# Kernel optimization log

Measured on AMD Instinct MI355X. Metric: run time of the kernel, lower is better.

## Reference

```python
import jax, jax.numpy as jnp
import numpy as np

EPS = 1e-12  # torch F.normalize default eps


def conv1x1(x, w, b):
    # x: [N,C,H,W], w: [O,C], b: [O]
    return jnp.einsum('nchw,oc->nohw', x, w) + b[None, :, None, None]


def forward_sa(f1, f2, cw1, cb1, cw2, cb2):
    c1 = conv1x1(f1, cw1, cb1)  # [N,1,H,W]
    c2 = conv1x1(f2, cw2, cb2)
    n, _, h, w = c1.shape
    c1 = jax.nn.softmax(c1.reshape(n, 1, h * w), axis=-1).reshape(n, 1, h, w)
    c2 = jax.nn.softmax(c2.reshape(n, 1, h * w), axis=-1).reshape(n, 1, h, w)
    return c1 * f1, c2 * f2


def l2_normalize_ch(x):
    # F.normalize(x): L2 over channel dim (dim=1), norm clamped to eps
    n = jnp.sqrt(jnp.sum(x * x, axis=1, keepdims=True))
    return x / jnp.maximum(n, EPS)


def forward_ca(f1, f2, pw1, pb1, pw2, pb2):
    N, C, H, W = f1.shape
    HW = H * W
    f1_cl = conv1x1(f1, pw1, pb1).reshape(N, -1, HW)  # [N,Cl,HW]
    f2_cl = conv1x1(f2, pw2, pb2).reshape(N, -1, HW)
    # A = f2_cl^T @ f1_cl : [N,HW,HW]
    A_c = jnp.tanh(jnp.einsum('nci,ncj->nij', f2_cl, f1_cl))
    f1_v = f1.reshape(N, C, HW)
    f2_v = f2.reshape(N, C, HW)
    # f1_hat = f1_v @ A_c^T ; f2_hat = f2_v @ A_c
    f1_hat = jnp.einsum('ncj,nij->nci', f1_v, A_c).reshape(N, C, H, W)
    f2_hat = jnp.einsum('ncj,nji->nci', f2_v, A_c).reshape(N, C, H, W)
    return l2_normalize_ch(f1_hat), l2_normalize_ch(f2_hat)


def setup_inputs() -> dict:
    key = jax.random.key(0)
    ks = jax.random.split(key, 10)
    N, C, H, W = 8, 256, 32, 32
    Cl = C // 16
    return {
        'f1': jax.random.normal(ks[0], (N, C, H, W), jnp.float32),
        'f2': jax.random.normal(ks[1], (N, C, H, W), jnp.float32),
        'pw1': jax.random.normal(ks[2], (Cl, C), jnp.float32) * 0.05,
        'pb1': jax.random.normal(ks[3], (Cl,), jnp.float32) * 0.05,
        'pw2': jax.random.normal(ks[4], (Cl, C), jnp.float32) * 0.05,
        'pb2': jax.random.normal(ks[5], (Cl,), jnp.float32) * 0.05,
        'cw1': jax.random.normal(ks[6], (1, C), jnp.float32) * 0.05,
        'cb1': jax.random.normal(ks[7], (1,), jnp.float32) * 0.05,
        'cw2': jax.random.normal(ks[8], (1, C), jnp.float32) * 0.05,
        'cb2': jax.random.normal(ks[9], (1,), jnp.float32) * 0.05,
    }


def reference(f1, f2, pw1, pb1, pw2, pb2, cw1, cb1, cw2, cb2):
    fp1, fp2 = f1, f2
    for i in range(5):
        s1, s2 = forward_sa(fp1, fp2, cw1, cb1, cw2, cb2)
        h1, h2 = forward_ca(s1, s2, pw1, pb1, pw2, pb2)
        if i < 4:
            fp1 = jax.nn.relu(h1 + fp1)
            fp2 = jax.nn.relu(h2 + fp2)
    return h1, h2, s1, s2
```

## Files before the change

### kernel.cpp

```cpp
#include <hip/hip_runtime.h>
#include <cstdint>
#include <cstddef>

#define N_  8
#define C_  256
#define HW_ 1024
#define CL_ 16
#define SZ_ (N_*C_*HW_)
#define WSCALE_ 4096.0f

typedef __attribute__((ext_vector_type(8))) _Float16 half8;
typedef __attribute__((ext_vector_type(4))) float f32x4;

static __device__ __forceinline__ float tanh_fast(float x){
  x = fminf(fmaxf(x, -15.f), 15.f);
  float e = __expf(2.f * x);
  return (e - 1.f) / (e + 1.f);
}

static __device__ __forceinline__ unsigned short f2h(float x){
  _Float16 h = (_Float16)x;
  return *(unsigned short*)&h;
}

static __device__ __forceinline__ void combine16(
    const float* __restrict__ mpart, const float* __restrict__ spart,
    int base, float& m, float& rl)
{
  m = -1e30f;
  #pragma unroll
  for (int k = 0; k < 16; ++k) m = fmaxf(m, mpart[base * 16 + k]);
  float s = 0.f;
  #pragma unroll
  for (int k = 0; k < 16; ++k) s += spart[base * 16 + k] * __expf(mpart[base * 16 + k] - m);
  rl = 1.f / s;
}

#define GLD16(g, l) __builtin_amdgcn_global_load_lds( \
    (const __attribute__((address_space(1))) void*)(g), \
    (__attribute__((address_space(3))) void*)(l), 16, 0, 0)

#define WAITV(N) asm volatile("s_waitcnt vmcnt(" #N ")" ::: "memory")

__global__ __launch_bounds__(256) void k_sa_dot(
    const float* __restrict__ fp1, const float* __restrict__ fp2,
    const float* __restrict__ cw1, const float* __restrict__ cw2,
    const float* __restrict__ pw1, const float* __restrict__ pw2,
    float* __restrict__ cval, float* __restrict__ pdot,
    float* __restrict__ mpart, float* __restrict__ spart,
    _Float16* __restrict__ fh1, _Float16* __restrict__ fh2)
{
  const int bid = blockIdx.x;
  const int n = bid & 7, r = bid >> 3;
  const int side = r >> 4, hw0 = (r & 15) * 64;
  const int t = threadIdx.x, hwl = t & 63, cg = t >> 6;
  const float* __restrict__ pw = side ? pw2 : pw1;
  const float* __restrict__ cw = side ? cw2 : cw1;
  const float* __restrict__ f  = (side ? fp2 : fp1) + (size_t)n * C_ * HW_ + hw0 + hwl;
  _Float16* __restrict__ fh = (side ? fh2 : fh1) + (size_t)n * C_ * HW_ + hw0 + hwl;
  const int cb = __builtin_amdgcn_readfirstlane(cg * 64);

  float acc[17];
  #pragma unroll
  for (int l = 0; l < 17; ++l) acc[l] = 0.f;

  for (int cc = 0; cc < 64; ++cc){
    const int c = cb + cc;
    const float v = f[(size_t)c * HW_];
    fh[(size_t)c * HW_] = (_Float16)v;
    acc[16] += v * cw[c];
    #pragma unroll
    for (int l = 0; l < 16; ++l) acc[l] += v * pw[l * C_ + c];
  }

  __shared__ float red[17][4][64];
  #pragma unroll
  for (int l = 0; l < 17; ++l) red[l][cg][hwl] = acc[l];
  __syncthreads();

  if (t < 64){
    const int base = n * 2 + side;
    float xc = 0.f;
    #pragma unroll
    for (int l = 0; l < 17; ++l){
      const float s = red[l][0][t] + red[l][1][t] + red[l][2][t] + red[l][3][t];
      if (l < 16) pdot[((size_t)base * CL_ + l) * HW_ + hw0 + t] = s;
      else      { cval[(size_t)base * HW_ + hw0 + t] = s; xc = s; }
    }
    float mb = xc;
    #pragma unroll
    for (int off = 32; off; off >>= 1) mb = fmaxf(mb, __shfl_xor(mb, off));
    float e = __expf(xc - mb);
    #pragma unroll
    for (int off = 32; off; off >>= 1) e += __shfl_xor(e, off);
    if (t == 0){
      mpart[base * 16 + (hw0 >> 6)] = mb;
      spart[base * 16 + (hw0 >> 6)] = e;
    }
  }
}

__global__ __launch_bounds__(256) void k_corr(
    const float* __restrict__ cval, const float* __restrict__ pdot,
    const float* __restrict__ pb1, const float* __restrict__ pb2,
    const float* __restrict__ mpart, const float* __restrict__ spart,
    unsigned short* __restrict__ Abf, unsigned short* __restrict__ Atbf)
{
  const int bid = blockIdx.x;
  const int n = bid & 7, r4i = bid >> 3;
  const int i0 = (r4i >> 4) * 64, j0 = (r4i & 15) * 64;
  const int b1 = n * 2, b2 = n * 2 + 1;
  __align__(16) __shared__ float s2[CL_][64];
  __align__(16) __shared__ float s1[CL_][64];
  __shared__ unsigned short at_s[64][68];
  const int t = threadIdx.x;
  const int lr = t >> 4, lc = (t & 15) * 4;

  float m1, rl1, m2, rl2;
  combine16(mpart, spart, b1, m1, rl1);
  combine16(mpart, spart, b2, m2, rl2);

  {
    const float bias2 = pb2[lr];
    const float4 c2 = *(const float4*)&cval[(size_t)b2 * HW_ + i0 + lc];
    const float4 p2 = *(const float4*)&pdot[((size_t)b2 * CL_ + lr) * HW_ + i0 + lc];
    s2[lr][lc + 0] = __expf(c2.x - m2) * rl2 * p2.x + bias2;
    s2[lr][lc + 1] = __expf(c2.y - m2) * rl2 * p2.y + bias2;
    s2[lr][lc + 2] = __expf(c2.z - m2) * rl2 * p2.z + bias2;
    s2[lr][lc + 3] = __expf(c2.w - m2) * rl2 * p2.w + bias2;

    const float bias1 = pb1[lr];
    const float4 c1 = *(const float4*)&cval[(size_t)b1 * HW_ + j0 + lc];
    const float4 p1 = *(const float4*)&pdot[((size_t)b1 * CL_ + lr) * HW_ + j0 + lc];
    s1[lr][lc + 0] = __expf(c1.x - m1) * rl1 * p1.x + bias1;
    s1[lr][lc + 1] = __expf(c1.y - m1) * rl1 * p1.y + bias1;
    s1[lr][lc + 2] = __expf(c1.z - m1) * rl1 * p1.z + bias1;
    s1[lr][lc + 3] = __expf(c1.w - m1) * rl1 * p1.w + bias1;
  }
  __syncthreads();

  const int ti = t >> 4, tj = t & 15;
  float acc[4][4];
  #pragma unroll
  for (int a = 0; a < 4; ++a)
    #pragma unroll
    for (int b = 0; b < 4; ++b) acc[a][b] = 0.f;

  #pragma unroll
  for (int l = 0; l < CL_; ++l){
    const float4 a4 = *(const float4*)&s2[l][ti * 4];
    const float4 b4 = *(const float4*)&s1[l][tj * 4];
    const float av[4] = {a4.x, a4.y, a4.z, a4.w};
    const float bv[4] = {b4.x, b4.y, b4.z, b4.w};
    #pragma unroll
    for (int a = 0; a < 4; ++a)
      #pragma unroll
      for (int b = 0; b < 4; ++b) acc[a][b] += av[a] * bv[b];
  }

  float tf[4][4];
  #pragma unroll
  for (int a = 0; a < 4; ++a)
    #pragma unroll
    for (int b = 0; b < 4; ++b) tf[a][b] = tanh_fast(acc[a][b]);

  float w1j[4], w2i[4];
  #pragma unroll
  for (int b = 0; b < 4; ++b)
    w1j[b] = WSCALE_ * __expf(cval[(size_t)b1 * HW_ + j0 + tj * 4 + b] - m1) * rl1;
  #pragma unroll
  for (int a = 0; a < 4; ++a)
    w2i[a] = WSCALE_ * __expf(cval[(size_t)b2 * HW_ + i0 + ti * 4 + a] - m2) * rl2;

  unsigned short* __restrict__ An  = Abf  + ((size_t)n << 20);
  unsigned short* __restrict__ Atn = Atbf + ((size_t)n << 20);
  #pragma unroll
  for (int a = 0; a < 4; ++a){
    ushort4 va;
    va.x = f2h(tf[a][0] * w1j[0]); va.y = f2h(tf[a][1] * w1j[1]);
    va.z = f2h(tf[a][2] * w1j[2]); va.w = f2h(tf[a][3] * w1j[3]);
    *(ushort4*)&An[(size_t)(i0 + ti * 4 + a) * HW_ + j0 + tj * 4] = va;
  }
  #pragma unroll
  for (int b = 0; b < 4; ++b){
    ushort4 vb;
    vb.x = f2h(tf[0][b] * w2i[0]); vb.y = f2h(tf[1][b] * w2i[1]);
    vb.z = f2h(tf[2][b] * w2i[2]); vb.w = f2h(tf[3][b] * w2i[3]);
    *(ushort4*)&at_s[tj * 4 + b][ti * 4] = vb;
  }
  __syncthreads();
  #pragma unroll
  for (int rep = 0; rep < 2; ++rep){
    const int idx = t + rep * 256;
    const int r = idx >> 3, q = (idx & 7) * 8;
    const ushort4 lo = *(const ushort4*)&at_s[r][q];
    const ushort4 hi = *(const ushort4*)&at_s[r][q + 4];
    *(ushort4*)&Atn[(size_t)(j0 + r) * HW_ + i0 + q] = lo;
    *(ushort4*)&Atn[(size_t)(j0 + r) * HW_ + i0 + q + 4] = hi;
  }
}

__global__ __launch_bounds__(512, 4) void k_gemm_fused(
    const _Float16* __restrict__ fhc1, const _Float16* __restrict__ fhc2,
    const unsigned short* __restrict__ Abf, const unsigned short* __restrict__ Atbf,
    const float* __restrict__ fpin1, const float* __restrict__ fpin2,
    float* __restrict__ fpo1, float* __restrict__ fpo2,
    _Float16* __restrict__ fhn1, _Float16* __restrict__ fhn2,
    const float* __restrict__ pw1, const float* __restrict__ pw2,
    const float* __restrict__ cw1, const float* __restrict__ cw2,
    float* __restrict__ cval, float* __restrict__ pdot,
    float* __restrict__ mpart, float* __restrict__ spart,
    float* __restrict__ out, int last)
{
  const int bid = blockIdx.x;
  const int n = bid & 7, r2 = bid >> 3;
  const int g = r2 >> 4, i0 = (r2 & 15) * 64;
  const unsigned short* __restrict__ X =
      (const unsigned short*)((g ? fhc2 : fhc1) + (size_t)n * C_ * HW_);
  const unsigned short* __restrict__ B = (g ? Atbf : Abf) + ((size_t)n << 20);

  __shared__ __align__(16) unsigned char pool[61440];

  const int t = threadIdx.x, w = t >> 6, l = t & 63;
  const int wr = w >> 1, wc = w & 1;

  f32x4 acc[4][2];
  #pragma unroll
  for (int fm = 0; fm < 4; ++fm)
    #pragma unroll
    for (int fn = 0; fn < 2; ++fn)
      acc[fm][fn] = (f32x4){0.f, 0.f, 0.f, 0.f};

  auto stage = [&](int buf, int k0){
    unsigned short* Xsb = (unsigned short*)(pool + buf * 16384);
    #pragma unroll
    for (int s = 0; s < 2; ++s){
      const int q = (w * 2 + s) * 64 + l;
      const int row = q >> 2;
      const int kc = (q & 3) ^ (row & 3);
      GLD16(X + (size_t)row * HW_ + k0 + kc * 8, &Xsb[(w * 2 + s) * 512]);
    }
    if (w < 4){
      unsigned short* Bsb = (unsigned short*)(pool + 49152 + buf * 4096);
      const int q = w * 64 + l;
      const int row = q >> 2;
      const int kc = (q & 3) ^ (row & 3);
      GLD16(B + (size_t)(i0 + row) * HW_ + k0 + kc * 8, &Bsb[w * 512]);
    }
  };

  stage(0, 0);
  stage(1, 32);
  stage(2, 64);

  int cur = 0;
  for (int kt = 0; kt < 32; ++kt){
    const int rem = (31 - kt) < 2 ? (31 - kt) : 2;
    if (w < 4){
      if (rem == 2)      WAITV(6);
      else if (rem == 1) WAITV(3);
      else               WAITV(0);
    } else {
      if (rem == 2)      WAITV(4);
      else if (rem == 1) WAITV(2);
      else               WAITV(0);
    }
    __builtin_amdgcn_sched_barrier(0);
    __builtin_amdgcn_s_barrier();

    const unsigned short* Xsb = (const unsigned short*)(pool + cur * 16384);
    const unsigned short* Bsb = (const unsigned short*)(pool + 49152 + cur * 4096);
    half8 a[4], bb[2];
    #pragma unroll
    for (int fm = 0; fm < 4; ++fm){
      const int row = wr * 64 + fm * 16 + (l & 15);
      const int kc = (l >> 4) ^ (row & 3);
      a[fm] = *(const half8*)&Xsb[row * 32 + kc * 8];
    }
    #pragma unroll
    for (int fn = 0; fn < 2; ++fn){
      const int row = wc * 32 + fn * 16 + (l & 15);
      const int kc = (l >> 4) ^ (row & 3);
      bb[fn] = *(const half8*)&Bsb[row * 32 + kc * 8];
    }
    #pragma unroll
    for (int fm = 0; fm < 4; ++fm)
      #pragma unroll
      for (int fn = 0; fn < 2; ++fn)
        acc[fm][fn] = __builtin_amdgcn_mfma_f32_16x16x32_f16(a[fm], bb[fn], acc[fm][fn], 0, 0, 0);

    asm volatile("s_waitcnt lgkmcnt(0)" ::: "memory");
    __builtin_amdgcn_sched_barrier(0);
    __builtin_amdgcn_s_barrier();
    __builtin_amdgcn_sched_barrier(0);

    if (kt < 29) stage(cur, (kt + 3) * 32);
    cur = (cur == 2) ? 0 : cur + 1;
  }

  float* pwT   = (float*)pool;
  float* redp  = (float*)(pool + 20480);
  float* ssred = (float*)(pool + 55296);
  float* rinvp = (float*)(pool + 56320);

  float ss0 = 0.f, ss1 = 0.f;
  #pragma unroll
  for (int fm = 0; fm < 4; ++fm)
    #pragma unroll
    for (int r = 0; r < 4; ++r){
      ss0 += acc[fm][0][r] * acc[fm][0][r];
      ss1 += acc[fm][1][r] * acc[fm][1][r];
    }
  ss0 += __shfl_xor(ss0, 16); ss0 += __shfl_xor(ss0, 32);
  ss1 += __shfl_xor(ss1, 16); ss1 += __shfl_xor(ss1, 32);
  if (l < 16){
    ssred[wr * 64 + wc * 32 + l]      = ss0;
    ssred[wr * 64 + wc * 32 + 16 + l] = ss1;
  }

  if (!last){
    const float* __restrict__ pw = g ? pw2 : pw1;
    const float* __restrict__ cw = g ? cw2 : cw1;
    {
      const int idx = t * 8;
      const int lq = idx >> 8, c = idx & 255;
      const float4 p0 = *(const float4*)&pw[lq * C_ + c];
      const float4 p1 = *(const float4*)&pw[lq * C_ + c + 4];
      pwT[(c + 0) * 20 + lq] = p0.x; pwT[(c + 1) * 20 + lq] = p0.y;
      pwT[(c + 2) * 20 + lq] = p0.z; pwT[(c + 3) * 20 + lq] = p0.w;
      pwT[(c + 4) * 20 + lq] = p1.x; pwT[(c + 5) * 20 + lq] = p1.y;
      pwT[(c + 6) * 20 + lq] = p1.z; pwT[(c + 7) * 20 + lq] = p1.w;
    }
    if (t < 32){
      const float4 c0 = *(const float4*)&cw[t * 8];
      const float4 c1 = *(const float4*)&cw[t * 8 + 4];
      pwT[(t * 8 + 0) * 20 + 16] = c0.x; pwT[(t * 8 + 1) * 20 + 16] = c0.y;
      pwT[(t * 8 + 2) * 20 + 16] = c0.z; pwT[(t * 8 + 3) * 20 + 16] = c0.w;
      pwT[(t * 8 + 4) * 20 + 16] = c1.x; pwT[(t * 8 + 5) * 20 + 16] = c1.y;
      pwT[(t * 8 + 6) * 20 + 16] = c1.z; pwT[(t * 8 + 7) * 20 + 16] = c1.w;
    }
  }
  __syncthreads();
  if (t < 64){
    const float s = ssred[t] + ssred[64 + t] + ssred[128 + t] + ssred[192 + t];
    rinvp[t] = 1.f / fmaxf(sqrtf(s), 1e-12f);
  }
  __syncthreads();
  const float ri[2] = { rinvp[wc * 32 + (l & 15)], rinvp[wc * 32 + 16 + (l & 15)] };

  const float* __restrict__ fpin = (g ? fpin2 : fpin1) + (size_t)n * C_ * HW_;
  float* __restrict__ fpo  = (g ? fpo2 : fpo1) + (size_t)n * C_ * HW_;
  _Float16* __restrict__ fhn = (g ? fhn2 : fhn1) + (size_t)n * C_ * HW_;
  float* __restrict__ outp = out + (size_t)g * SZ_ + (size_t)n * C_ * HW_;
  const int rbase = (l >> 4) * 4, col = l & 15;
  const int baseio = n * 2 + g;

  if (!last){
    float sacc[2][17];
    #pragma unroll
    for (int fn = 0; fn < 2; ++fn)
      #pragma unroll
      for (int lq = 0; lq < 17; ++lq) sacc[fn][lq] = 0.f;

    #pragma unroll
    for (int fm = 0; fm < 4; ++fm)
      #pragma unroll
      for (int r = 0; r < 4; ++r){
        const int c = wr * 64 + fm * 16 + rbase + r;
        float prow[17];
        #pragma unroll
        for (int q4 = 0; q4 < 4; ++q4){
          const float4 pv = *(const float4*)&pwT[c * 20 + q4 * 4];
          prow[q4 * 4 + 0] = pv.x; prow[q4 * 4 + 1] = pv.y;
          prow[q4 * 4 + 2] = pv.z; prow[q4 * 4 + 3] = pv.w;
        }
        prow[16] = pwT[c * 20 + 16];
        #pragma unroll
        for (int fn = 0; fn < 2; ++fn){
          const size_t base = (size_t)c * HW_ + i0 + wc * 32 + fn * 16 + col;
          const float h = acc[fm][fn][r] * ri[fn];
          const float fv = fpin[base] + h;
          const float rv = fv > 0.f ? fv : 0.f;
          fpo[base] = rv;
          fhn[base] = (_Float16)rv;
          #pragma unroll
          for (int lq = 0; lq < 17; ++lq) sacc[fn][lq] += rv * prow[lq];
        }
      }

    #pragma unroll
    for (int fn = 0; fn < 2; ++fn)
      #pragma unroll
      for (int lq = 0; lq < 17; ++lq){
        float v = sacc[fn][lq];
        v += __shfl_xor(v, 16);
        v += __shfl_xor(v, 32);
        sacc[fn][lq] = v;
      }
    if (l < 16){
      #pragma unroll
      for (int fn = 0; fn < 2; ++fn)
        #pragma unroll
        for (int lq = 0; lq < 17; ++lq)
          redp[(((wr * 2 + wc) * 2 + fn) * 17 + lq) * 16 + l] = sacc[fn][lq];
    }
    __syncthreads();
    if (t < 64){
      const int wcx = t >> 5, fnx = (t >> 4) & 1, colx = t & 15;
      float xc = 0.f;
      #pragma unroll
      for (int lq = 0; lq < 17; ++lq){
        float s = 0.f;
        #pragma unroll
        for (int wrx = 0; wrx < 4; ++wrx)
          s += redp[(((wrx * 2 + wcx) * 2 + fnx) * 17 + lq) * 16 + colx];
        if (lq < 16) pdot[((size_t)baseio * CL_ + lq) * HW_ + i0 + t] = s;
        else       { cval[(size_t)baseio * HW_ + i0 + t] = s; xc = s; }
      }
      float mb = xc;
      #pragma unroll
      for (int off = 32; off; off >>= 1) mb = fmaxf(mb, __shfl_xor(mb, off));
      float e = __expf(xc - mb);
      #pragma unroll
      for (int off = 32; off; off >>= 1) e += __shfl_xor(e, off);
      if (t == 0){
        mpart[baseio * 16 + (i0 >> 6)] = mb;
        spart[baseio * 16 + (i0 >> 6)] = e;
      }
    }
  } else {
    #pragma unroll
    for (int fm = 0; fm < 4; ++fm)
      #pragma unroll
      for (int fn = 0; fn < 2; ++fn){
        const size_t base = (size_t)(wr * 64 + fm * 16 + rbase) * HW_ + i0 + wc * 32 + fn * 16 + col;
        #pragma unroll
        for (int r = 0; r < 4; ++r)
          outp[base + (size_t)r * HW_] = acc[fm][fn][r] * ri[fn];
      }
  }
}

__global__ __launch_bounds__(256) void k_s_out(
    const float* __restrict__ fp1, const float* __restrict__ fp2,
    const float* __restrict__ cval,
    const float* __restrict__ mpart, const float* __restrict__ spart,
    float* __restrict__ out)
{
  const int side = blockIdx.y;
  const size_t fo = ((size_t)blockIdx.x * 256 + threadIdx.x) * 4;
  const float* __restrict__ f = side ? fp2 : fp1;
  const int n  = (int)(fo >> 18);
  const int hw = (int)(fo & (HW_ - 1));
  const int base = n * 2 + side;
  float m, rl;
  combine16(mpart, spart, base, m, rl);
  const float4 c = *(const float4*)&cval[(size_t)base * HW_ + hw];
  const float4 v = *(const float4*)&f[fo];
  float4 r;
  r.x = v.x * (__expf(c.x - m) * rl);
  r.y = v.y * (__expf(c.y - m) * rl);
  r.z = v.z * (__expf(c.z - m) * rl);
  r.w = v.w * (__expf(c.w - m) * rl);
  *(float4*)&out[(size_t)(2 + side) * SZ_ + fo] = r;
}

extern "C" void kernel_launch(void* const* d_in, const int* in_sizes, int n_in,
                              void* d_out, int out_size, void* d_ws, size_t ws_size,
                              hipStream_t stream)
{
  const float* f1  = (const float*)d_in[0];
  const float* f2  = (const float*)d_in[1];
  const float* pw1 = (const float*)d_in[2];
  const float* pb1 = (const float*)d_in[3];
  const float* pw2 = (const float*)d_in[4];
  const float* pb2 = (const float*)d_in[5];
  const float* cw1 = (const float*)d_in[6];
  const float* cw2 = (const float*)d_in[8];
  float* out = (float*)d_out;
  float* ws  = (float*)d_ws;

  float* cval  = ws;
  float* pdot  = cval + N_ * 2 * HW_;
  float* mpart = pdot + N_ * 2 * CL_ * HW_;
  float* spart = mpart + 512;
  float* fp1   = spart + 512;
  float* fp2   = fp1 + SZ_;
  _Float16* fhA1 = (_Float16*)(fp2 + SZ_);
  _Float16* fhA2 = fhA1 + SZ_;
  _Float16* fhB1 = fhA2 + SZ_;
  _Float16* fhB2 = fhB1 + SZ_;
  unsigned short* Abf  = (unsigned short*)(fhB2 + SZ_);
  unsigned short* Atbf = Abf + ((size_t)N_ << 20);

  k_sa_dot<<<dim3(256), 256, 0, stream>>>(f1, f2, cw1, cw2, pw1, pw2,
                                          cval, pdot, mpart, spart, fhA1, fhA2);

  for (int it = 0; it < 5; ++it){
    const float* cur1 = (it == 0) ? f1 : fp1;
    const float* cur2 = (it == 0) ? f2 : fp2;
    const _Float16* fhc1 = (it & 1) ? fhB1 : fhA1;
    const _Float16* fhc2 = (it & 1) ? fhB2 : fhA2;
    _Float16* fhn1 = (it & 1) ? fhA1 : fhB1;
    _Float16* fhn2 = (it & 1) ? fhA2 : fhB2;

    k_corr<<<dim3(2048), 256, 0, stream>>>(cval, pdot, pb1, pb2, mpart, spart, Abf, Atbf);
    if (it == 4)
      k_s_out<<<dim3(SZ_ / 4 / 256, 2), 256, 0, stream>>>(cur1, cur2, cval, mpart, spart, out);
    k_gemm_fused<<<dim3(256), 512, 0, stream>>>(fhc1, fhc2, Abf, Atbf,
                                                cur1, cur2, fp1, fp2, fhn1, fhn2,
                                                pw1, pw2, cw1, cw2,
                                                cval, pdot, mpart, spart,
                                                out, (it == 4) ? 1 : 0);
  }
}
```

Measured before the change: 236.7 us.

## Split GEMM K dimension in two and move epilogue into separate finish kernel

Result: slower. 286.9 us (+21.2%).

```diff
diff --git a/kernel.cpp b/kernel.cpp
--- a/kernel.cpp
+++ b/kernel.cpp
@@ -200,9 +200,118 @@
   }
 }
 
-__global__ __launch_bounds__(512, 4) void k_gemm_fused(
+__global__ __launch_bounds__(512, 4) void k_gemm_split(
     const _Float16* __restrict__ fhc1, const _Float16* __restrict__ fhc2,
     const unsigned short* __restrict__ Abf, const unsigned short* __restrict__ Atbf,
+    float* __restrict__ ppart)
+{
+  const int bid = blockIdx.x;
+  const int n = bid & 7;
+  const int b2 = bid >> 3;
+  const int kh = b2 & 1;
+  const int it = (b2 >> 1) & 15;
+  const int g  = b2 >> 5;
+  const int i0 = it * 64;
+  const int kbase = kh * 512;
+
+  const unsigned short* __restrict__ X =
+      (const unsigned short*)((g ? fhc2 : fhc1) + (size_t)n * C_ * HW_);
+  const unsigned short* __restrict__ B = (g ? Atbf : Abf) + ((size_t)n << 20);
+
+  __shared__ __align__(16) unsigned char pool[61440];
+
+  const int t = threadIdx.x, w = t >> 6, l = t & 63;
+  const int wr = w >> 1, wc = w & 1;
+
+  f32x4 acc[4][2];
+  #pragma unroll
+  for (int fm = 0; fm < 4; ++fm)
+    #pragma unroll
+    for (int fn = 0; fn < 2; ++fn)
+      acc[fm][fn] = (f32x4){0.f, 0.f, 0.f, 0.f};
+
+  auto stage = [&](int buf, int k0){
+    unsigned short* Xsb = (unsigned short*)(pool + buf * 16384);
+    #pragma unroll
+    for (int s = 0; s < 2; ++s){
+      const int q = (w * 2 + s) * 64 + l;
+      const int row = q >> 2;
+      const int kc = (q & 3) ^ (row & 3);
+      GLD16(X + (size_t)row * HW_ + k0 + kc * 8, &Xsb[(w * 2 + s) * 512]);
+    }
+    if (w < 4){
+      unsigned short* Bsb = (unsigned short*)(pool + 49152 + buf * 4096);
+      const int q = w * 64 + l;
+      const int row = q >> 2;
+      const int kc = (q & 3) ^ (row & 3);
+      GLD16(B + (size_t)(i0 + row) * HW_ + k0 + kc * 8, &Bsb[w * 512]);
+    }
+  };
+
+  stage(0, kbase);
+  stage(1, kbase + 32);
+  stage(2, kbase + 64);
+
+  int cur = 0;
+  for (int kt = 0; kt < 16; ++kt){
+    const int rem = (15 - kt) < 2 ? (15 - kt) : 2;
+    if (w < 4){
+      if (rem == 2)      WAITV(6);
+      else if (rem == 1) WAITV(3);
+      else               WAITV(0);
+    } else {
+      if (rem == 2)      WAITV(4);
+      else if (rem == 1) WAITV(2);
+      else               WAITV(0);
+    }
+    __builtin_amdgcn_sched_barrier(0);
+    __builtin_amdgcn_s_barrier();
+
+    const unsigned short* Xsb = (const unsigned short*)(pool + cur * 16384);
+    const unsigned short* Bsb = (const unsigned short*)(pool + 49152 + cur * 4096);
+    half8 a[4], bb[2];
+    #pragma unroll
+    for (int fm = 0; fm < 4; ++fm){
+      const int row = wr * 64 + fm * 16 + (l & 15);
+      const int kc = (l >> 4) ^ (row & 3);
+      a[fm] = *(const half8*)&Xsb[row * 32 + kc * 8];
+    }
+    #pragma unroll
+    for (int fn = 0; fn < 2; ++fn){
+      const int row = wc * 32 + fn * 16 + (l & 15);
+      const int kc = (l >> 4) ^ (row & 3);
+      bb[fn] = *(const half8*)&Bsb[row * 32 + kc * 8];
+    }
+    #pragma unroll
+    for (int fm = 0; fm < 4; ++fm)
+      #pragma unroll
+      for (int fn = 0; fn < 2; ++fn)
+        acc[fm][fn] = __builtin_amdgcn_mfma_f32_16x16x32_f16(a[fm], bb[fn], acc[fm][fn], 0, 0, 0);
+
+    asm volatile("s_waitcnt lgkmcnt(0)" ::: "memory");
+    __builtin_amdgcn_sched_barrier(0);
+    __builtin_amdgcn_s_barrier();
+    __builtin_amdgcn_sched_barrier(0);
+
+    if (kt < 13) stage(cur, kbase + (kt + 3) * 32);
+    cur = (cur == 2) ? 0 : cur + 1;
+  }
+
+  float* __restrict__ pp = ppart + (((size_t)(n * 2 + g) * 2 + kh) * C_) * HW_;
+  const int rbase = (l >> 4) * 4, col = l & 15;
+  #pragma unroll
+  for (int fm = 0; fm < 4; ++fm)
+    #pragma unroll
+    for (int fn = 0; fn < 2; ++fn){
+      const size_t base = (size_t)(wr * 64 + fm * 16 + rbase) * HW_ + i0 + wc * 32 + fn * 16 + col;
+      #pragma unroll
+      for (int r = 0; r < 4; ++r)
+        pp[base + (size_t)r * HW_] = acc[fm][fn][r];
+    }
+}
+
+__global__ __launch_bounds__(512, 4) void k_finish(
+    const float* __restrict__ ppart,
     const float* __restrict__ fpin1, const float* __restrict__ fpin2,
     float* __restrict__ fpo1, float* __restrict__ fpo2,
     _Float16* __restrict__ fhn1, _Float16* __restrict__ fhn2,
@@ -215,93 +324,30 @@
   const int bid = blockIdx.x;
   const int n = bid & 7, r2 = bid >> 3;
   const int g = r2 >> 4, i0 = (r2 & 15) * 64;
-  const unsigned short* __restrict__ X =
-      (const unsigned short*)((g ? fhc2 : fhc1) + (size_t)n * C_ * HW_);
-  const unsigned short* __restrict__ B = (g ? Atbf : Abf) + ((size_t)n << 20);
-
-  __shared__ __align__(16) unsigned char pool[61440];
+
+  __shared__ __align__(16) unsigned char pool[40960];
+  float* pwT   = (float*)pool;
+  float* redp  = (float*)(pool + 20480);
+  float* ssred = (float*)(pool + 37888);
+  float* rinvp = (float*)(pool + 38912);
 
   const int t = threadIdx.x, w = t >> 6, l = t & 63;
   const int wr = w >> 1, wc = w & 1;
+  const int rbase = (l >> 4) * 4, col = l & 15;
+
+  const float* __restrict__ pp0 = ppart + (((size_t)(n * 2 + g) * 2 + 0) * C_) * HW_;
+  const float* __restrict__ pp1 = pp0 + (size_t)C_ * HW_;
 
   f32x4 acc[4][2];
   #pragma unroll
   for (int fm = 0; fm < 4; ++fm)
     #pragma unroll
-    for (int fn = 0; fn < 2; ++fn)
-      acc[fm][fn] = (f32x4){0.f, 0.f, 0.f, 0.f};
-
-  auto stage = [&](int buf, int k0){
-    unsigned short* Xsb = (unsigned short*)(pool + buf * 16384);
-    #pragma unroll
-    for (int s = 0; s < 2; ++s){
-      const int q = (w * 2 + s) * 64 + l;
-      const int row = q >> 2;
-      const int kc = (q & 3) ^ (row & 3);
-      GLD16(X + (size_t)row * HW_ + k0 + kc * 8, &Xsb[(w * 2 + s) * 512]);
-    }
-    if (w < 4){
-      unsigned short* Bsb = (unsigned short*)(pool + 49152 + buf * 4096);
-      const int q = w * 64 + l;
-      const int row = q >> 2;
-      const int kc = (q & 3) ^ (row & 3);
-      GLD16(B + (size_t)(i0 + row) * HW_ + k0 + kc * 8, &Bsb[w * 512]);
-    }
-  };
-
-  stage(0, 0);
-  stage(1, 32);
-  stage(2, 64);
-
-  int cur = 0;
-  for (int kt = 0; kt < 32; ++kt){
-    const int rem = (31 - kt) < 2 ? (31 - kt) : 2;
-    if (w < 4){
-      if (rem == 2)      WAITV(6);
-      else if (rem == 1) WAITV(3);
-      else               WAITV(0);
-    } else {
-      if (rem == 2)      WAITV(4);
-      else if (rem == 1) WAITV(2);
-      else               WAITV(0);
-    }
-    __builtin_amdgcn_sched_barrier(0);
-    __builtin_amdgcn_s_barrier();
-
-    const unsigned short* Xsb = (const unsigned short*)(pool + cur * 16384);
-    const unsigned short* Bsb = (const unsigned short*)(pool + 49152 + cur * 4096);
-    half8 a[4], bb[2];
-    #pragma unroll
-    for (int fm = 0; fm < 4; ++fm){
-      const int row = wr * 64 + fm * 16 + (l & 15);
-      const int kc = (l >> 4) ^ (row & 3);
-      a[fm] = *(const half8*)&Xsb[row * 32 + kc * 8];
-    }
-    #pragma unroll
     for (int fn = 0; fn < 2; ++fn){
-      const int row = wc * 32 + fn * 16 + (l & 15);
-      const int kc = (l >> 4) ^ (row & 3);
-      bb[fn] = *(const half8*)&Bsb[row * 32 + kc * 8];
-    }
-    #pragma unroll
-    for (int fm = 0; fm < 4; ++fm)
-      #pragma unroll
-      for (int fn = 0; fn < 2; ++fn)
-        acc[fm][fn] = __builtin_amdgcn_mfma_f32_16x16x32_f16(a[fm], bb[fn], acc[fm][fn], 0, 0, 0);
-
-    asm volatile("s_waitcnt lgkmcnt(0)" ::: "memory");
-    __builtin_amdgcn_sched_barrier(0);
-    __builtin_amdgcn_s_barrier();
-    __builtin_amdgcn_sched_barrier(0);
-
-    if (kt < 29) stage(cur, (kt + 3) * 32);
-    cur = (cur == 2) ? 0 : cur + 1;
-  }
-
-  float* pwT   = (float*)pool;
-  float* redp  = (float*)(pool + 20480);
-  float* ssred = (float*)(pool + 55296);
-  float* rinvp = (float*)(pool + 56320);
+      const size_t base = (size_t)(wr * 64 + fm * 16 + rbase) * HW_ + i0 + wc * 32 + fn * 16 + col;
+      #pragma unroll
+      for (int r = 0; r < 4; ++r)
+        acc[fm][fn][r] = pp0[base + (size_t)r * HW_] + pp1[base + (size_t)r * HW_];
+    }
 
   float ss0 = 0.f, ss1 = 0.f;
   #pragma unroll
@@ -352,7 +398,6 @@
   float* __restrict__ fpo  = (g ? fpo2 : fpo1) + (size_t)n * C_ * HW_;
   _Float16* __restrict__ fhn = (g ? fhn2 : fhn1) + (size_t)n * C_ * HW_;
   float* __restrict__ outp = out + (size_t)g * SZ_ + (size_t)n * C_ * HW_;
-  const int rbase = (l >> 4) * 4, col = l & 15;
   const int baseio = n * 2 + g;
 
   if (!last){
@@ -492,6 +537,7 @@
   _Float16* fhB2 = fhB1 + SZ_;
   unsigned short* Abf  = (unsigned short*)(fhB2 + SZ_);
   unsigned short* Atbf = Abf + ((size_t)N_ << 20);
+  float* ppart = (float*)(Atbf + ((size_t)N_ << 20));
 
   k_sa_dot<<<dim3(256), 256, 0, stream>>>(f1, f2, cw1, cw2, pw1, pw2,
                                           cval, pdot, mpart, spart, fhA1, fhA2);
@@ -507,10 +553,10 @@
     k_corr<<<dim3(2048), 256, 0, stream>>>(cval, pdot, pb1, pb2, mpart, spart, Abf, Atbf);
     if (it == 4)
       k_s_out<<<dim3(SZ_ / 4 / 256, 2), 256, 0, stream>>>(cur1, cur2, cval, mpart, spart, out);
-    k_gemm_fused<<<dim3(256), 512, 0, stream>>>(fhc1, fhc2, Abf, Atbf,
-                                                cur1, cur2, fp1, fp2, fhn1, fhn2,
-                                                pw1, pw2, cw1, cw2,
-                                                cval, pdot, mpart, spart,
-                                                out, (it == 4) ? 1 : 0);
-  }
-}
+    k_gemm_split<<<dim3(512), 512, 0, stream>>>(fhc1, fhc2, Abf, Atbf, ppart);
+    k_finish<<<dim3(256), 512, 0, stream>>>(ppart, cur1, cur2, fp1, fp2, fhn1, fhn2,
+                                            pw1, pw2, cw1, cw2,
+                                            cval, pdot, mpart, spart,
+                                            out, (it == 4) ? 1 : 0);
+  }
+}
```
